# Optimization experiments

Measured on AMD Instinct MI355X. Metric: run time of the kernel, lower is better.

Reference implementation:

```python
import jax, jax.numpy as jnp
import numpy as np

T, B, I, H, FC, C = 256, 256, 1024, 256, 128, 8  # seq, batch, input, hidden, fc1, classes


def setup_inputs() -> dict:
    key = jax.random.key(0)
    ks = jax.random.split(key, 9)
    s_ih = 1.0 / np.sqrt(H)
    return {
        "x": jax.random.normal(ks[0], (T, B, I), dtype=jnp.float32),
        "W_ih": jax.random.uniform(ks[1], (4 * H, I), jnp.float32, -s_ih, s_ih),
        "W_hh": jax.random.uniform(ks[2], (4 * H, H), jnp.float32, -s_ih, s_ih),
        "b_ih": jax.random.uniform(ks[3], (4 * H,), jnp.float32, -s_ih, s_ih),
        "b_hh": jax.random.uniform(ks[4], (4 * H,), jnp.float32, -s_ih, s_ih),
        "W1": jax.random.uniform(ks[5], (FC, H), jnp.float32, -s_ih, s_ih),
        "b1": jax.random.uniform(ks[6], (FC,), jnp.float32, -s_ih, s_ih),
        "W2": jax.random.uniform(ks[7], (C, FC), jnp.float32, -1.0 / np.sqrt(FC), 1.0 / np.sqrt(FC)),
        "b2": jax.random.uniform(ks[8], (C,), jnp.float32, -1.0 / np.sqrt(FC), 1.0 / np.sqrt(FC)),
    }


def _lstm(x, W_ih, W_hh, b_ih, b_hh):
    # x: [T, B, I]; PyTorch gate order: i, f, g, o
    xg = jnp.einsum("tbi,gi->tbg", x, W_ih) + b_ih + b_hh  # precompute input projections [T,B,4H]

    def step(carry, xg_t):
        h, c = carry
        z = xg_t + h @ W_hh.T  # [B, 4H]
        i, f, g, o = jnp.split(z, 4, axis=-1)
        i = jax.nn.sigmoid(i)
        f = jax.nn.sigmoid(f)
        g = jnp.tanh(g)
        o = jax.nn.sigmoid(o)
        c = f * c + i * g
        h = o * jnp.tanh(c)
        return (h, c), h

    h0 = jnp.zeros((x.shape[1], W_hh.shape[1]), x.dtype)
    (hn, cn), out = jax.lax.scan(step, (h0, h0), xg)
    return out  # [T, B, H]


def reference(x, W_ih, W_hh, b_ih, b_hh, W1, b1, W2, b2):
    out = _lstm(x, W_ih, W_hh, b_ih, b_hh)      # [T, B, H]
    out = jax.nn.relu(out)
    out = jax.nn.relu(out @ W1.T + b1)           # [T, B, 128]
    out = out @ W2.T + b2                        # [T, B, num_classes]
    return out
```

## Files before the change

kernel.cpp:

```cpp
#include <hip/hip_runtime.h>
#include <type_traits>


typedef float    f4    __attribute__((ext_vector_type(4)));
typedef float    f32x4 __attribute__((ext_vector_type(4)));
typedef _Float16 h8    __attribute__((ext_vector_type(8)));
typedef _Float16 h4    __attribute__((ext_vector_type(4)));

__device__ __forceinline__ float ldf(const float* p)    { return *p; }
__device__ __forceinline__ float ldf(const _Float16* p) { return (float)*p; }

__device__ __forceinline__ float fast_sigmoid(float x) {
    return 1.f / (1.f + __expf(-x));
}
__device__ __forceinline__ float fast_tanh(float x) {
    const float e = __expf(-2.f * fabsf(x));
    const float t = (1.f - e) / (1.f + e);
    return copysignf(t, x);
}

__global__ __launch_bounds__(256) void k_bias(const float* __restrict__ b_ih,
                                              const float* __restrict__ b_hh,
                                              float* __restrict__ bias) {
    const int i = blockIdx.x * 256 + threadIdx.x;
    if (i < 1024) bias[i] = b_ih[i] + b_hh[i];
}

__global__ __launch_bounds__(256) void k_pack(const float* __restrict__ W_hh,
                                              _Float16* __restrict__ Wp) {
    const int idx = blockIdx.x * 256 + threadIdx.x;
    const int fi = idx >> 6;
    const int l  = idx & 63;
    const int g  = (fi >> 3) * 16 + (l & 15);
    const int k  = (fi & 7) * 32 + ((l >> 4) << 3);
    const float* src = &W_hh[(size_t)g * 256 + k];
    h8 v;
    #pragma unroll
    for (int c = 0; c < 8; ++c) v[c] = (_Float16)src[c];
    *(h8*)&Wp[(size_t)idx * 8] = v;
}

__global__ __launch_bounds__(256) void k_xg_mfma(
    const float* __restrict__ x, const float* __restrict__ W_ih,
    const float* __restrict__ bias, _Float16* __restrict__ xg2)
{
    __shared__ _Float16 As[2][128][40];
    __shared__ _Float16 Bs[2][128][40];
    const int tid = threadIdx.x;
    const int l   = tid & 63;
    const int w   = tid >> 6;
    const int m0  = blockIdx.y * 128;
    const int n0  = blockIdx.x * 128;
    const int wr  = (w >> 1) * 64;
    const int wc  = (w & 1) * 64;
    const int srow = tid >> 2;
    const int skof = (tid & 3) * 8;
    const int lr = l & 15;
    const int lg = l >> 4;

    f32x4 acc[4][4] = {};
    f4 ldA[2][2], ldB[2][2];

    auto XG_LOAD = [&](int kt) {
        const int k0 = kt * 32;
        #pragma unroll
        for (int s = 0; s < 2; ++s) {
            const float* xa = &x[(size_t)(m0 + srow + s * 64) * 1024 + k0 + skof];
            const float* wb = &W_ih[(size_t)(n0 + srow + s * 64) * 1024 + k0 + skof];
            ldA[s][0] = *(const f4*)xa; ldA[s][1] = *(const f4*)(xa + 4);
            ldB[s][0] = *(const f4*)wb; ldB[s][1] = *(const f4*)(wb + 4);
        }
    };
    auto XG_WRITE = [&](int buf) {
        #pragma unroll
        for (int s = 0; s < 2; ++s) {
            h8 va, vb;
            #pragma unroll
            for (int c = 0; c < 8; ++c) {
                va[c] = (_Float16)ldA[s][c >> 2][c & 3];
                vb[c] = (_Float16)ldB[s][c >> 2][c & 3];
            }
            *(h8*)&As[buf][srow + s * 64][skof] = va;
            *(h8*)&Bs[buf][srow + s * 64][skof] = vb;
        }
    };

    XG_LOAD(0);
    XG_WRITE(0);
    __syncthreads();
    for (int kt = 0; kt < 32; ++kt) {
        const int cur = kt & 1;
        if (kt + 1 < 32) XG_LOAD(kt + 1);
        h8 af[4], bf[4];
        #pragma unroll
        for (int mf = 0; mf < 4; ++mf) af[mf] = *(const h8*)&As[cur][wr + mf * 16 + lr][lg * 8];
        #pragma unroll
        for (int nf = 0; nf < 4; ++nf) bf[nf] = *(const h8*)&Bs[cur][wc + nf * 16 + lr][lg * 8];
        #pragma unroll
        for (int mf = 0; mf < 4; ++mf)
            #pragma unroll
            for (int nf = 0; nf < 4; ++nf)
                acc[mf][nf] = __builtin_amdgcn_mfma_f32_16x16x32_f16(af[mf], bf[nf], acc[mf][nf], 0, 0, 0);
        if (kt + 1 < 32) XG_WRITE((kt + 1) & 1);
        __syncthreads();
    }
    #pragma unroll
    for (int nf = 0; nf < 4; ++nf) {
        const int col  = n0 + wc + nf * 16 + lr;
        const float bv = bias[col];
        const int gate = col >> 8;
        const int njp  = col & 255;
        const int wt   = njp >> 6;
        const int jt   = (njp >> 4) & 3;
        #pragma unroll
        for (int mf = 0; mf < 4; ++mf) {
            const int rowb = m0 + wr + mf * 16 + lg * 4;
            const int tt = rowb >> 8;
            const int gb = (rowb >> 4) & 15;
            h4 pk;
            #pragma unroll
            for (int r = 0; r < 4; ++r) pk[r] = (_Float16)(acc[mf][nf][r] + bv);
            *(h4*)&xg2[((((size_t)tt * 16 + gb) * 4 + wt) * 64 + l) * 64 + gate * 16 + jt * 4] = pk;
        }
    }
}

__global__ __launch_bounds__(256, 1) void k_lstm_reg(
    const _Float16* __restrict__ xg2, const _Float16* __restrict__ Wp,
    _Float16* __restrict__ h_all)
{
    __shared__ _Float16 wlds[4 * 34 * 512];
    __shared__ _Float16 h_sh[2][16][264];
    const int tid = threadIdx.x;
    const int w  = tid >> 6;
    const int l  = tid & 63;
    const int lr = l & 15;
    const int lg = l >> 4;
    const int g  = blockIdx.x;
    const int b0 = g * 16;

    auto fgid = [&](int ti, int kb) {
        return (((ti >> 2) * 16 + w * 4 + (ti & 3)) * 8 + kb);
    };

    h8 Wreg[84];
    #pragma unroll
    for (int kb = 0; kb < 5; ++kb)
        #pragma unroll
        for (int ti = 0; ti < 16; ++ti)
            Wreg[kb * 16 + ti] = *(const h8*)&Wp[((size_t)fgid(ti, kb) * 64 + l) * 8];
    #pragma unroll
    for (int ti = 0; ti < 4; ++ti)
        Wreg[80 + ti] = *(const h8*)&Wp[((size_t)fgid(ti, 5) * 64 + l) * 8];

    #pragma unroll
    for (int ti = 4; ti < 16; ++ti) {
        const h8 v = *(const h8*)&Wp[((size_t)fgid(ti, 5) * 64 + l) * 8];
        *(h8*)&wlds[((w * 34 + (ti - 4)) * 64 + l) * 8] = v;
    }
    #pragma unroll
    for (int ti = 0; ti < 14; ++ti) {
        const h8 v = *(const h8*)&Wp[((size_t)fgid(ti, 6) * 64 + l) * 8];
        *(h8*)&wlds[((w * 34 + (12 + ti)) * 64 + l) * 8] = v;
    }
    #pragma unroll
    for (int ti = 0; ti < 8; ++ti) {
        const h8 v = *(const h8*)&Wp[((size_t)fgid(ti, 7) * 64 + l) * 8];
        *(h8*)&wlds[((w * 34 + (26 + ti)) * 64 + l) * 8] = v;
    }

    {
        _Float16* p = &h_sh[0][0][0];
        for (int i = tid; i < 2 * 16 * 264; i += 256) p[i] = (_Float16)0.f;
    }
    __syncthreads();

    float c[16];
    #pragma unroll
    for (int i = 0; i < 16; ++i) c[i] = 0.f;

    for (int t = 0; t < 256; ++t) {
        const int cur = t & 1;
        const int nxt = cur ^ 1;

        const size_t E = ((((size_t)t * 16 + g) * 4 + w) * 64 + l) * 64;
        h8 xqv[8];
        #pragma unroll
        for (int q = 0; q < 8; ++q) xqv[q] = *(const h8*)&xg2[E + q * 8];

        unsigned soff = 0;
        asm volatile("" : "+v"(soff));
        h8 sv[10];
        #pragma unroll
        for (int s2 = 0; s2 < 8; ++s2)
            sv[s2] = *(const h8*)&Wp[((size_t)fgid(8 + s2, 7) * 64 + l) * 8 + soff];
        sv[8] = *(const h8*)&Wp[((size_t)fgid(14, 6) * 64 + l) * 8 + soff];
        sv[9] = *(const h8*)&Wp[((size_t)fgid(15, 6) * 64 + l) * 8 + soff];

        f32x4 acc[16] = {};

        h8 ab[2];
        ab[0] = *(const h8*)&h_sh[cur][lr][0 * 32 + lg * 8];
        ab[1] = *(const h8*)&h_sh[cur][lr][1 * 32 + lg * 8];

        #pragma unroll
        for (int kb = 0; kb < 8; ++kb) {
            const h8 av = ab[kb & 1];
            #pragma unroll
            for (int ti = 0; ti < 16; ++ti) {
                h8 b;
                if (kb <= 4)                  b = Wreg[kb * 16 + ti];
                else if (kb == 5 && ti < 4)   b = Wreg[80 + ti];
                else if (kb == 5)             b = *(const h8*)&wlds[((w * 34 + (ti - 4)) * 64 + l) * 8];
                else if (kb == 6 && ti < 14)  b = *(const h8*)&wlds[((w * 34 + (12 + ti)) * 64 + l) * 8];
                else if (kb == 6)             b = sv[8 + (ti - 14)];
                else if (ti < 8)              b = *(const h8*)&wlds[((w * 34 + (26 + ti)) * 64 + l) * 8];
                else                          b = sv[ti - 8];
                acc[ti] = __builtin_amdgcn_mfma_f32_16x16x32_f16(av, b, acc[ti], 0, 0, 0);
            }
            if (kb + 2 < 8)
                ab[kb & 1] = *(const h8*)&h_sh[cur][lr][(kb + 2) * 32 + lg * 8];
        }

        #pragma unroll
        for (int jt = 0; jt < 4; ++jt) {
            #pragma unroll
            for (int r = 0; r < 4; ++r) {
                const int v0 = 0 * 16 + jt * 4 + r;
                const int v1 = 1 * 16 + jt * 4 + r;
                const int v2 = 2 * 16 + jt * 4 + r;
                const int v3 = 3 * 16 + jt * 4 + r;
                const float zi = acc[0 * 4 + jt][r] + (float)xqv[v0 >> 3][v0 & 7];
                const float zf = acc[1 * 4 + jt][r] + (float)xqv[v1 >> 3][v1 & 7];
                const float zg = acc[2 * 4 + jt][r] + (float)xqv[v2 >> 3][v2 & 7];
                const float zo = acc[3 * 4 + jt][r] + (float)xqv[v3 >> 3][v3 & 7];
                const float ig = fast_sigmoid(zi);
                const float fg = fast_sigmoid(zf);
                const float gg = fast_tanh(zg);
                const float og = fast_sigmoid(zo);
                const int ci = jt * 4 + r;
                c[ci] = fg * c[ci] + ig * gg;
                const float hv = og * fast_tanh(c[ci]);
                const _Float16 h16 = (_Float16)hv;
                h_sh[nxt][lg * 4 + r][w * 64 + jt * 16 + lr] = h16;
                h_all[((size_t)t * 256 + b0 + lg * 4 + r) * 256 + w * 64 + jt * 16 + lr] = h16;
            }
        }
        __syncthreads();
    }
}

template <typename HT>
__global__ __launch_bounds__(256) void k_fc(
    const HT* __restrict__ h_all, const float* __restrict__ W1,
    const float* __restrict__ b1, const float* __restrict__ W2,
    const float* __restrict__ b2, float* __restrict__ out)
{
    __shared__ __align__(16) float smem[12288];
    float* hsT = smem;
    float* w1T = smem + 4096;
    const int tid = threadIdx.x;
    const int m0 = blockIdx.x * 64;
    const int tx = tid & 15;
    const int ty = tid >> 4;
    const int r0 = ty * 4;
    const int fA = tx * 4;
    const int fB = 64 + tx * 4;
    float acc[4][8] = {};
    for (int kc = 0; kc < 4; ++kc) {
        const int k0 = kc * 64;
        __syncthreads();
        #pragma unroll
        for (int i = 0; i < 4; ++i) {
            const int fid = tid + i * 256;
            const int rr = fid >> 4;
            const int qq = fid & 15;
            const HT* p = &h_all[(size_t)(m0 + rr) * 256 + k0 + qq * 4];
            f4 v;
            if constexpr (std::is_same<HT, float>::value) {
                v = *(const f4*)p;
            } else {
                v[0] = ldf(p); v[1] = ldf(p + 1); v[2] = ldf(p + 2); v[3] = ldf(p + 3);
            }
            #pragma unroll
            for (int cc = 0; cc < 4; ++cc)
                hsT[(qq * 4 + cc) * 64 + rr] = fmaxf(v[cc], 0.f);
        }
        #pragma unroll
        for (int i = 0; i < 8; ++i) {
            const int fid = tid + i * 256;
            const int ff = fid >> 4;
            const int qq = fid & 15;
            const f4 v = *(const f4*)&W1[(size_t)ff * 256 + k0 + qq * 4];
            #pragma unroll
            for (int cc = 0; cc < 4; ++cc)
                w1T[(qq * 4 + cc) * 128 + ff] = v[cc];
        }
        __syncthreads();
        #pragma unroll 4
        for (int kk = 0; kk < 64; ++kk) {
            const f4 aa = *(const f4*)&hsT[kk * 64 + r0];
            const f4 ba = *(const f4*)&w1T[kk * 128 + fA];
            const f4 bb = *(const f4*)&w1T[kk * 128 + fB];
            #pragma unroll
            for (int i = 0; i < 4; ++i) {
                #pragma unroll
                for (int j = 0; j < 4; ++j) {
                    acc[i][j]     = fmaf(aa[i], ba[j], acc[i][j]);
                    acc[i][j + 4] = fmaf(aa[i], bb[j], acc[i][j + 4]);
                }
            }
        }
    }
    __syncthreads();
    float* fc1s = smem;
    #pragma unroll
    for (int j = 0; j < 4; ++j) {
        const float bbA = b1[fA + j];
        const float bbB = b1[fB + j];
        #pragma unroll
        for (int i = 0; i < 4; ++i) {
            fc1s[(r0 + i) * 132 + fA + j] = fmaxf(acc[i][j] + bbA, 0.f);
            fc1s[(r0 + i) * 132 + fB + j] = fmaxf(acc[i][j + 4] + bbB, 0.f);
        }
    }
    __syncthreads();
    const int r  = tid >> 2;
    const int c0 = (tid & 3) * 2;
    float o0 = b2[c0], o1 = b2[c0 + 1];
    #pragma unroll
    for (int fq = 0; fq < 32; ++fq) {
        const f4 p  = *(const f4*)&fc1s[r * 132 + fq * 4];
        const f4 wa = *(const f4*)&W2[(size_t)c0 * 128 + fq * 4];
        const f4 wb = *(const f4*)&W2[(size_t)(c0 + 1) * 128 + fq * 4];
        o0 += p[0] * wa[0] + p[1] * wa[1] + p[2] * wa[2] + p[3] * wa[3];
        o1 += p[0] * wb[0] + p[1] * wb[1] + p[2] * wb[2] + p[3] * wb[3];
    }
    out[(size_t)(m0 + r) * 8 + c0]     = o0;
    out[(size_t)(m0 + r) * 8 + c0 + 1] = o1;
}

extern "C" void kernel_launch(void* const* d_in, const int* in_sizes, int n_in,
                              void* d_out, int out_size, void* d_ws, size_t ws_size,
                              hipStream_t stream)
{
    const float* x    = (const float*)d_in[0];
    const float* W_ih = (const float*)d_in[1];
    const float* W_hh = (const float*)d_in[2];
    const float* b_ih = (const float*)d_in[3];
    const float* b_hh = (const float*)d_in[4];
    const float* W1   = (const float*)d_in[5];
    const float* b1   = (const float*)d_in[6];
    const float* W2   = (const float*)d_in[7];
    const float* b2   = (const float*)d_in[8];
    float* out = (float*)d_out;
    char* ws = (char*)d_ws;

    _Float16* xg2   = (_Float16*)ws;
    _Float16* h_all = (_Float16*)(ws + 134217728);
    _Float16* Wp    = (_Float16*)(ws + 167772160);
    float*    bias  = (float*)   (ws + 168296448);

    k_bias<<<4, 256, 0, stream>>>(b_ih, b_hh, bias);
    k_pack<<<128, 256, 0, stream>>>(W_hh, Wp);
    k_xg_mfma<<<dim3(8, 512), 256, 0, stream>>>(x, W_ih, bias, xg2);
    k_lstm_reg<<<16, 256, 0, stream>>>(xg2, Wp, h_all);
    k_fc<_Float16><<<1024, 256, 0, stream>>>(h_all, W1, b1, W2, b2, out);
}
```

Baseline: 2.217 ms.

## Hold recurrent weights in AGPRs via inline-asm MFMA and preload xg into accumulators

Rewrites the serial LSTM recurrence kernel so that 63 W_hh fragments live in accumulation registers (AGPRs) and are fed to MFMA directly as the B operand through inline asm. This frees VGPRs, so more fragments stay in registers and fewer are read from LDS or re-read from global memory on every timestep. The precomputed input projection is also loaded into the accumulators before the MFMA chain, which removes the separate add in the gate epilogue. The risk is that the inline asm constraints cause compiler-inserted copies or spills, and LDS use grows slightly.

```diff
diff --git a/kernel.cpp b/kernel.cpp
--- a/kernel.cpp
+++ b/kernel.cpp
@@ -17,6 +17,11 @@
     const float e = __expf(-2.f * fabsf(x));
     const float t = (1.f - e) / (1.f + e);
     return copysignf(t, x);
+}
+
+__device__ __forceinline__ void mfma_agpr(f32x4& acc, h8 a, const f32x4& b) {
+    asm("v_mfma_f32_16x16x32_f16 %0, %1, %2, %0"
+        : "+v"(acc) : "v"(a), "a"(b));
 }
 
 __global__ __launch_bounds__(256) void k_bias(const float* __restrict__ b_ih,
@@ -125,11 +130,11 @@
     }
 }
 
-__global__ __launch_bounds__(256, 1) void k_lstm_reg(
+__global__ __launch_bounds__(256, 1) void k_lstm_agpr(
     const _Float16* __restrict__ xg2, const _Float16* __restrict__ Wp,
     _Float16* __restrict__ h_all)
 {
-    __shared__ _Float16 wlds[4 * 34 * 512];
+    __shared__ _Float16 wlds[4 * 35 * 512];
     __shared__ _Float16 h_sh[2][16][264];
     const int tid = threadIdx.x;
     const int w  = tid >> 6;
@@ -142,32 +147,36 @@
     auto fgid = [&](int ti, int kb) {
         return (((ti >> 2) * 16 + w * 4 + (ti & 3)) * 8 + kb);
     };
-
-    h8 Wreg[84];
-    #pragma unroll
-    for (int kb = 0; kb < 5; ++kb)
+    auto ldfrag = [&](int ti, int kb) {
+        return *(const h8*)&Wp[((size_t)fgid(ti, kb) * 64 + l) * 8];
+    };
+
+    f32x4 wag[63];
+    #pragma unroll
+    for (int kb = 0; kb < 3; ++kb)
         #pragma unroll
         for (int ti = 0; ti < 16; ++ti)
-            Wreg[kb * 16 + ti] = *(const h8*)&Wp[((size_t)fgid(ti, kb) * 64 + l) * 8];
-    #pragma unroll
-    for (int ti = 0; ti < 4; ++ti)
-        Wreg[80 + ti] = *(const h8*)&Wp[((size_t)fgid(ti, 5) * 64 + l) * 8];
-
-    #pragma unroll
-    for (int ti = 4; ti < 16; ++ti) {
-        const h8 v = *(const h8*)&Wp[((size_t)fgid(ti, 5) * 64 + l) * 8];
-        *(h8*)&wlds[((w * 34 + (ti - 4)) * 64 + l) * 8] = v;
-    }
-    #pragma unroll
-    for (int ti = 0; ti < 14; ++ti) {
-        const h8 v = *(const h8*)&Wp[((size_t)fgid(ti, 6) * 64 + l) * 8];
-        *(h8*)&wlds[((w * 34 + (12 + ti)) * 64 + l) * 8] = v;
-    }
-    #pragma unroll
-    for (int ti = 0; ti < 8; ++ti) {
-        const h8 v = *(const h8*)&Wp[((size_t)fgid(ti, 7) * 64 + l) * 8];
-        *(h8*)&wlds[((w * 34 + (26 + ti)) * 64 + l) * 8] = v;
-    }
+            wag[kb * 16 + ti] = __builtin_bit_cast(f32x4, ldfrag(ti, kb));
+    #pragma unroll
+    for (int ti = 0; ti < 15; ++ti)
+        wag[48 + ti] = __builtin_bit_cast(f32x4, ldfrag(ti, 3));
+
+    h8 wvg[21];
+    wvg[0] = ldfrag(15, 3);
+    #pragma unroll
+    for (int ti = 0; ti < 16; ++ti) wvg[1 + ti] = ldfrag(ti, 4);
+    #pragma unroll
+    for (int ti = 0; ti < 4; ++ti) wvg[17 + ti] = ldfrag(ti, 7);
+
+    #pragma unroll
+    for (int ti = 0; ti < 16; ++ti)
+        *(h8*)&wlds[((w * 35 + ti) * 64 + l) * 8] = ldfrag(ti, 5);
+    #pragma unroll
+    for (int ti = 0; ti < 16; ++ti)
+        *(h8*)&wlds[((w * 35 + 16 + ti) * 64 + l) * 8] = ldfrag(ti, 6);
+    #pragma unroll
+    for (int ti = 4; ti < 7; ++ti)
+        *(h8*)&wlds[((w * 35 + 32 + (ti - 4)) * 64 + l) * 8] = ldfrag(ti, 7);
 
     {
         _Float16* p = &h_sh[0][0][0];
@@ -188,35 +197,52 @@
         #pragma unroll
         for (int q = 0; q < 8; ++q) xqv[q] = *(const h8*)&xg2[E + q * 8];
 
-        unsigned soff = 0;
-        asm volatile("" : "+v"(soff));
-        h8 sv[10];
-        #pragma unroll
-        for (int s2 = 0; s2 < 8; ++s2)
-            sv[s2] = *(const h8*)&Wp[((size_t)fgid(8 + s2, 7) * 64 + l) * 8 + soff];
-        sv[8] = *(const h8*)&Wp[((size_t)fgid(14, 6) * 64 + l) * 8 + soff];
-        sv[9] = *(const h8*)&Wp[((size_t)fgid(15, 6) * 64 + l) * 8 + soff];
-
-        f32x4 acc[16] = {};
-
         h8 ab[2];
         ab[0] = *(const h8*)&h_sh[cur][lr][0 * 32 + lg * 8];
         ab[1] = *(const h8*)&h_sh[cur][lr][1 * 32 + lg * 8];
 
+        f32x4 acc[16];
+        #pragma unroll
+        for (int ti = 0; ti < 16; ++ti) {
+            #pragma unroll
+            for (int r = 0; r < 4; ++r) {
+                const int v = (ti >> 2) * 16 + (ti & 3) * 4 + r;
+                acc[ti][r] = (float)xqv[v >> 3][v & 7];
+            }
+        }
+
+        unsigned soff = 0;
+        asm volatile("" : "+v"(soff));
+        h8 sv[9];
+        #pragma unroll
+        for (int s2 = 0; s2 < 9; ++s2)
+            sv[s2] = *(const h8*)&Wp[((size_t)fgid(7 + s2, 7) * 64 + l) * 8 + soff];
+
         #pragma unroll
         for (int kb = 0; kb < 8; ++kb) {
             const h8 av = ab[kb & 1];
             #pragma unroll
             for (int ti = 0; ti < 16; ++ti) {
-                h8 b;
-                if (kb <= 4)                  b = Wreg[kb * 16 + ti];
-                else if (kb == 5 && ti < 4)   b = Wreg[80 + ti];
-                else if (kb == 5)             b = *(const h8*)&wlds[((w * 34 + (ti - 4)) * 64 + l) * 8];
-                else if (kb == 6 && ti < 14)  b = *(const h8*)&wlds[((w * 34 + (12 + ti)) * 64 + l) * 8];
-                else if (kb == 6)             b = sv[8 + (ti - 14)];
-                else if (ti < 8)              b = *(const h8*)&wlds[((w * 34 + (26 + ti)) * 64 + l) * 8];
-                else                          b = sv[ti - 8];
-                acc[ti] = __builtin_amdgcn_mfma_f32_16x16x32_f16(av, b, acc[ti], 0, 0, 0);
+                if (kb < 3) {
+                    mfma_agpr(acc[ti], av, wag[kb * 16 + ti]);
+                } else if (kb == 3) {
+                    if (ti < 15) mfma_agpr(acc[ti], av, wag[48 + ti]);
+                    else acc[ti] = __builtin_amdgcn_mfma_f32_16x16x32_f16(av, wvg[0], acc[ti], 0, 0, 0);
+                } else if (kb == 4) {
+                    acc[ti] = __builtin_amdgcn_mfma_f32_16x16x32_f16(av, wvg[1 + ti], acc[ti], 0, 0, 0);
+                } else if (kb == 5) {
+                    const h8 b = *(const h8*)&wlds[((w * 35 + ti) * 64 + l) * 8];
+                    acc[ti] = __builtin_amdgcn_mfma_f32_16x16x32_f16(av, b, acc[ti], 0, 0, 0);
+                } else if (kb == 6) {
+                    const h8 b = *(const h8*)&wlds[((w * 35 + 16 + ti) * 64 + l) * 8];
+                    acc[ti] = __builtin_amdgcn_mfma_f32_16x16x32_f16(av, b, acc[ti], 0, 0, 0);
+                } else {
+                    h8 b;
+                    if (ti < 4)      b = wvg[17 + ti];
+                    else if (ti < 7) b = *(const h8*)&wlds[((w * 35 + 32 + (ti - 4)) * 64 + l) * 8];
+                    else             b = sv[ti - 7];
+                    acc[ti] = __builtin_amdgcn_mfma_f32_16x16x32_f16(av, b, acc[ti], 0, 0, 0);
+                }
             }
             if (kb + 2 < 8)
                 ab[kb & 1] = *(const h8*)&h_sh[cur][lr][(kb + 2) * 32 + lg * 8];
@@ -226,18 +252,10 @@
         for (int jt = 0; jt < 4; ++jt) {
             #pragma unroll
             for (int r = 0; r < 4; ++r) {
-                const int v0 = 0 * 16 + jt * 4 + r;
-                const int v1 = 1 * 16 + jt * 4 + r;
-                const int v2 = 2 * 16 + jt * 4 + r;
-                const int v3 = 3 * 16 + jt * 4 + r;
-                const float zi = acc[0 * 4 + jt][r] + (float)xqv[v0 >> 3][v0 & 7];
-                const float zf = acc[1 * 4 + jt][r] + (float)xqv[v1 >> 3][v1 & 7];
-                const float zg = acc[2 * 4 + jt][r] + (float)xqv[v2 >> 3][v2 & 7];
-                const float zo = acc[3 * 4 + jt][r] + (float)xqv[v3 >> 3][v3 & 7];
-                const float ig = fast_sigmoid(zi);
-                const float fg = fast_sigmoid(zf);
-                const float gg = fast_tanh(zg);
-                const float og = fast_sigmoid(zo);
+                const float ig = fast_sigmoid(acc[0 * 4 + jt][r]);
+                const float fg = fast_sigmoid(acc[1 * 4 + jt][r]);
+                const float gg = fast_tanh(acc[2 * 4 + jt][r]);
+                const float og = fast_sigmoid(acc[3 * 4 + jt][r]);
                 const int ci = jt * 4 + r;
                 c[ci] = fg * c[ci] + ig * gg;
                 const float hv = og * fast_tanh(c[ci]);
@@ -364,6 +382,6 @@
     k_bias<<<4, 256, 0, stream>>>(b_ih, b_hh, bias);
     k_pack<<<128, 256, 0, stream>>>(W_hh, Wp);
     k_xg_mfma<<<dim3(8, 512), 256, 0, stream>>>(x, W_ih, bias, xg2);
-    k_lstm_reg<<<16, 256, 0, stream>>>(xg2, Wp, h_all);
+    k_lstm_agpr<<<16, 256, 0, stream>>>(xg2, Wp, h_all);
     k_fc<_Float16><<<1024, 256, 0, stream>>>(h_all, W1, b1, W2, b2, out);
 }
```

New measurement: 2.086 ms. 5.9% less time.

## Split LSTM recurrence across eight waves per block with rebalanced weight residency

Applied to the files above, without the earlier changes.

The recurrent kernel now runs 512 threads (8 waves) per batch group instead of 4, so each wave handles half as many hidden columns. W_hh fragments are redistributed: fewer are held in registers, some sit in LDS, and more are re-read from global memory (L2) every step. The xg layout is changed to match the 8-wave split, and xg is preloaded into the MFMA accumulators rather than added after. The aim is more MFMA parallelism per CU on the latency-bound serial chain, at the cost of more per-step global weight traffic.

```diff
diff --git a/kernel.cpp b/kernel.cpp
--- a/kernel.cpp
+++ b/kernel.cpp
@@ -109,9 +109,8 @@
         const int col  = n0 + wc + nf * 16 + lr;
         const float bv = bias[col];
         const int gate = col >> 8;
-        const int njp  = col & 255;
-        const int wt   = njp >> 6;
-        const int jt   = (njp >> 4) & 3;
+        const int w8   = (col >> 5) & 7;
+        const int jt   = (col >> 4) & 1;
         #pragma unroll
         for (int mf = 0; mf < 4; ++mf) {
             const int rowb = m0 + wr + mf * 16 + lg * 4;
@@ -120,16 +119,16 @@
             h4 pk;
             #pragma unroll
             for (int r = 0; r < 4; ++r) pk[r] = (_Float16)(acc[mf][nf][r] + bv);
-            *(h4*)&xg2[((((size_t)tt * 16 + gb) * 4 + wt) * 64 + l) * 64 + gate * 16 + jt * 4] = pk;
-        }
-    }
-}
-
-__global__ __launch_bounds__(256, 1) void k_lstm_reg(
+            *(h4*)&xg2[((((size_t)tt * 16 + gb) * 8 + w8) * 64 + l) * 32 + gate * 8 + jt * 4] = pk;
+        }
+    }
+}
+
+__global__ __launch_bounds__(512, 2) void k_lstm_8w(
     const _Float16* __restrict__ xg2, const _Float16* __restrict__ Wp,
     _Float16* __restrict__ h_all)
 {
-    __shared__ _Float16 wlds[4 * 34 * 512];
+    __shared__ _Float16 wlds[8 * 17 * 512];
     __shared__ _Float16 h_sh[2][16][264];
     const int tid = threadIdx.x;
     const int w  = tid >> 6;
@@ -140,110 +139,98 @@
     const int b0 = g * 16;
 
     auto fgid = [&](int ti, int kb) {
-        return (((ti >> 2) * 16 + w * 4 + (ti & 3)) * 8 + kb);
+        return (((ti >> 1) * 16 + w * 2 + (ti & 1)) * 8 + kb);
     };
-
-    h8 Wreg[84];
-    #pragma unroll
-    for (int kb = 0; kb < 5; ++kb)
-        #pragma unroll
-        for (int ti = 0; ti < 16; ++ti)
-            Wreg[kb * 16 + ti] = *(const h8*)&Wp[((size_t)fgid(ti, kb) * 64 + l) * 8];
-    #pragma unroll
-    for (int ti = 0; ti < 4; ++ti)
-        Wreg[80 + ti] = *(const h8*)&Wp[((size_t)fgid(ti, 5) * 64 + l) * 8];
-
-    #pragma unroll
-    for (int ti = 4; ti < 16; ++ti) {
-        const h8 v = *(const h8*)&Wp[((size_t)fgid(ti, 5) * 64 + l) * 8];
-        *(h8*)&wlds[((w * 34 + (ti - 4)) * 64 + l) * 8] = v;
-    }
-    #pragma unroll
-    for (int ti = 0; ti < 14; ++ti) {
-        const h8 v = *(const h8*)&Wp[((size_t)fgid(ti, 6) * 64 + l) * 8];
-        *(h8*)&wlds[((w * 34 + (12 + ti)) * 64 + l) * 8] = v;
-    }
-    #pragma unroll
-    for (int ti = 0; ti < 8; ++ti) {
-        const h8 v = *(const h8*)&Wp[((size_t)fgid(ti, 7) * 64 + l) * 8];
-        *(h8*)&wlds[((w * 34 + (26 + ti)) * 64 + l) * 8] = v;
-    }
+    auto ldfrag = [&](int ti, int kb) {
+        return *(const h8*)&Wp[((size_t)fgid(ti, kb) * 64 + l) * 8];
+    };
+
+    h8 wvg[24];
+    #pragma unroll
+    for (int kb = 0; kb < 3; ++kb)
+        #pragma unroll
+        for (int ti = 0; ti < 8; ++ti)
+            wvg[kb * 8 + ti] = ldfrag(ti, kb);
+
+    #pragma unroll
+    for (int ti = 0; ti < 8; ++ti)
+        *(h8*)&wlds[((w * 17 + ti) * 64 + l) * 8] = ldfrag(ti, 3);
+    #pragma unroll
+    for (int ti = 0; ti < 8; ++ti)
+        *(h8*)&wlds[((w * 17 + 8 + ti) * 64 + l) * 8] = ldfrag(ti, 4);
+    *(h8*)&wlds[((w * 17 + 16) * 64 + l) * 8] = ldfrag(0, 5);
 
     {
         _Float16* p = &h_sh[0][0][0];
-        for (int i = tid; i < 2 * 16 * 264; i += 256) p[i] = (_Float16)0.f;
+        for (int i = tid; i < 2 * 16 * 264; i += 512) p[i] = (_Float16)0.f;
     }
     __syncthreads();
 
-    float c[16];
-    #pragma unroll
-    for (int i = 0; i < 16; ++i) c[i] = 0.f;
+    float c[8];
+    #pragma unroll
+    for (int i = 0; i < 8; ++i) c[i] = 0.f;
 
     for (int t = 0; t < 256; ++t) {
         const int cur = t & 1;
         const int nxt = cur ^ 1;
 
-        const size_t E = ((((size_t)t * 16 + g) * 4 + w) * 64 + l) * 64;
-        h8 xqv[8];
-        #pragma unroll
-        for (int q = 0; q < 8; ++q) xqv[q] = *(const h8*)&xg2[E + q * 8];
+        const size_t E = ((((size_t)t * 16 + g) * 8 + w) * 64 + l) * 32;
+        h8 xq[4];
+        #pragma unroll
+        for (int q = 0; q < 4; ++q) xq[q] = *(const h8*)&xg2[E + q * 8];
 
         unsigned soff = 0;
         asm volatile("" : "+v"(soff));
-        h8 sv[10];
-        #pragma unroll
-        for (int s2 = 0; s2 < 8; ++s2)
-            sv[s2] = *(const h8*)&Wp[((size_t)fgid(8 + s2, 7) * 64 + l) * 8 + soff];
-        sv[8] = *(const h8*)&Wp[((size_t)fgid(14, 6) * 64 + l) * 8 + soff];
-        sv[9] = *(const h8*)&Wp[((size_t)fgid(15, 6) * 64 + l) * 8 + soff];
-
-        f32x4 acc[16] = {};
-
-        h8 ab[2];
-        ab[0] = *(const h8*)&h_sh[cur][lr][0 * 32 + lg * 8];
-        ab[1] = *(const h8*)&h_sh[cur][lr][1 * 32 + lg * 8];
+        h8 sv[23];
+        #pragma unroll
+        for (int ti = 1; ti < 8; ++ti)
+            sv[ti - 1] = *(const h8*)&Wp[((size_t)fgid(ti, 5) * 64 + l) * 8 + soff];
+        #pragma unroll
+        for (int ti = 0; ti < 8; ++ti)
+            sv[7 + ti] = *(const h8*)&Wp[((size_t)fgid(ti, 6) * 64 + l) * 8 + soff];
+        #pragma unroll
+        for (int ti = 0; ti < 8; ++ti)
+            sv[15 + ti] = *(const h8*)&Wp[((size_t)fgid(ti, 7) * 64 + l) * 8 + soff];
+
+        f32x4 acc[8];
+        #pragma unroll
+        for (int ti = 0; ti < 8; ++ti) {
+            #pragma unroll
+            for (int r = 0; r < 4; ++r)
+                acc[ti][r] = (float)xq[ti >> 1][(ti & 1) * 4 + r];
+        }
 
         #pragma unroll
         for (int kb = 0; kb < 8; ++kb) {
-            const h8 av = ab[kb & 1];
-            #pragma unroll
-            for (int ti = 0; ti < 16; ++ti) {
+            const h8 av = *(const h8*)&h_sh[cur][lr][kb * 32 + lg * 8];
+            #pragma unroll
+            for (int ti = 0; ti < 8; ++ti) {
                 h8 b;
-                if (kb <= 4)                  b = Wreg[kb * 16 + ti];
-                else if (kb == 5 && ti < 4)   b = Wreg[80 + ti];
-                else if (kb == 5)             b = *(const h8*)&wlds[((w * 34 + (ti - 4)) * 64 + l) * 8];
-                else if (kb == 6 && ti < 14)  b = *(const h8*)&wlds[((w * 34 + (12 + ti)) * 64 + l) * 8];
-                else if (kb == 6)             b = sv[8 + (ti - 14)];
-                else if (ti < 8)              b = *(const h8*)&wlds[((w * 34 + (26 + ti)) * 64 + l) * 8];
-                else                          b = sv[ti - 8];
+                if (kb < 3)                  b = wvg[kb * 8 + ti];
+                else if (kb == 3)            b = *(const h8*)&wlds[((w * 17 + ti) * 64 + l) * 8];
+                else if (kb == 4)            b = *(const h8*)&wlds[((w * 17 + 8 + ti) * 64 + l) * 8];
+                else if (kb == 5 && ti == 0) b = *(const h8*)&wlds[((w * 17 + 16) * 64 + l) * 8];
+                else if (kb == 5)            b = sv[ti - 1];
+                else if (kb == 6)            b = sv[7 + ti];
+                else                         b = sv[15 + ti];
                 acc[ti] = __builtin_amdgcn_mfma_f32_16x16x32_f16(av, b, acc[ti], 0, 0, 0);
             }
-            if (kb + 2 < 8)
-                ab[kb & 1] = *(const h8*)&h_sh[cur][lr][(kb + 2) * 32 + lg * 8];
-        }
-
-        #pragma unroll
-        for (int jt = 0; jt < 4; ++jt) {
+        }
+
+        #pragma unroll
+        for (int jt = 0; jt < 2; ++jt) {
             #pragma unroll
             for (int r = 0; r < 4; ++r) {
-                const int v0 = 0 * 16 + jt * 4 + r;
-                const int v1 = 1 * 16 + jt * 4 + r;
-                const int v2 = 2 * 16 + jt * 4 + r;
-                const int v3 = 3 * 16 + jt * 4 + r;
-                const float zi = acc[0 * 4 + jt][r] + (float)xqv[v0 >> 3][v0 & 7];
-                const float zf = acc[1 * 4 + jt][r] + (float)xqv[v1 >> 3][v1 & 7];
-                const float zg = acc[2 * 4 + jt][r] + (float)xqv[v2 >> 3][v2 & 7];
-                const float zo = acc[3 * 4 + jt][r] + (float)xqv[v3 >> 3][v3 & 7];
-                const float ig = fast_sigmoid(zi);
-                const float fg = fast_sigmoid(zf);
-                const float gg = fast_tanh(zg);
-                const float og = fast_sigmoid(zo);
+                const float ig = fast_sigmoid(acc[0 * 2 + jt][r]);
+                const float fg = fast_sigmoid(acc[1 * 2 + jt][r]);
+                const float gg = fast_tanh(acc[2 * 2 + jt][r]);
+                const float og = fast_sigmoid(acc[3 * 2 + jt][r]);
                 const int ci = jt * 4 + r;
                 c[ci] = fg * c[ci] + ig * gg;
                 const float hv = og * fast_tanh(c[ci]);
                 const _Float16 h16 = (_Float16)hv;
-                h_sh[nxt][lg * 4 + r][w * 64 + jt * 16 + lr] = h16;
-                h_all[((size_t)t * 256 + b0 + lg * 4 + r) * 256 + w * 64 + jt * 16 + lr] = h16;
+                h_sh[nxt][lg * 4 + r][w * 32 + jt * 16 + lr] = h16;
+                h_all[((size_t)t * 256 + b0 + lg * 4 + r) * 256 + w * 32 + jt * 16 + lr] = h16;
             }
         }
         __syncthreads();
@@ -364,6 +351,6 @@
     k_bias<<<4, 256, 0, stream>>>(b_ih, b_hh, bias);
     k_pack<<<128, 256, 0, stream>>>(W_hh, Wp);
     k_xg_mfma<<<dim3(8, 512), 256, 0, stream>>>(x, W_ih, bias, xg2);
-    k_lstm_reg<<<16, 256, 0, stream>>>(xg2, Wp, h_all);
+    k_lstm_8w<<<16, 512, 0, stream>>>(xg2, Wp, h_all);
     k_fc<_Float16><<<1024, 256, 0, stream>>>(h_all, W1, b1, W2, b2, out);
 }
```

After: 1.996 ms. -9.9%, faster.
